# Optimization experiments

Measured on AMD Instinct MI355X. Metric: run time of the kernel, lower is better.

Reference implementation:

```python
import jax, jax.numpy as jnp
import numpy as np

T, N, H, G = 4, 100000, 128, 1024
LN2 = float(np.log(2.0))
EPS = 1e-5


def ssp(x):
    # shifted softplus: softplus(x) - softplus(0)
    return jax.nn.softplus(x) - LN2


def layernorm(x, g, b):
    m = jnp.mean(x, axis=-1, keepdims=True)
    v = jnp.var(x, axis=-1, keepdims=True)
    return (x - m) * jax.lax.rsqrt(v + EPS) * g + b


def mlp3(x, Ws, bs, gs, bts):
    # 3 stacked Linear -> LayerNorm -> SSP stages
    for i in range(3):
        x = ssp(layernorm(x @ Ws[i] + bs[i], gs[i], bts[i]))
    return x


def setup_inputs() -> dict:
    key = jax.random.key(0)
    ks = jax.random.split(key, 8)
    s = 1.0 / np.sqrt(H)
    batch = jnp.sort((jnp.arange(N, dtype=jnp.int64) * G) // N).astype(jnp.int32)
    return {
        "x_proc": jax.random.normal(ks[0], (T, N, H), jnp.float32),
        "x_enc": jax.random.normal(ks[1], (N, H), jnp.float32),
        "batch": batch,
        "pW": jax.random.normal(ks[2], (3, H, H), jnp.float32) * s,
        "pb": jnp.zeros((3, H), jnp.float32),
        "pg": jnp.ones((3, H), jnp.float32),
        "pbt": jnp.zeros((3, H), jnp.float32),
        "eW": jax.random.normal(ks[3], (3, H, H), jnp.float32) * s,
        "eb": jnp.zeros((3, H), jnp.float32),
        "eg": jnp.ones((3, H), jnp.float32),
        "ebt": jnp.zeros((3, H), jnp.float32),
        "wp": jax.random.normal(ks[4], (H, 1), jnp.float32) * s,
        "bp": jnp.zeros((1,), jnp.float32),
        "we": jax.random.normal(ks[5], (H, 1), jnp.float32) * s,
        "be": jnp.zeros((1,), jnp.float32),
    }


def reference(x_proc, x_enc, batch, pW, pb, pg, pbt, eW, eb, eg, ebt, wp, bp, we, be):
    h_proc = mlp3(x_proc, pW, pb, pg, pbt)          # [T, N, H]
    h_enc = mlp3(x_enc, eW, eb, eg, ebt)            # [N, H]
    seg = lambda z: jax.ops.segment_sum(z, batch, num_segments=G)
    pooled_proc = jax.vmap(seg)(h_proc)             # [T, G, H]
    pooled_enc = seg(h_enc)                         # [G, H]
    target = pooled_proc @ wp + bp + (pooled_enc @ we + be)[None]  # [T, G, 1]
    return target.reshape(-1, G)                    # [T, G]
```

## Files before the change

### kernel.cpp

```cpp
#include <hip/hip_runtime.h>
#include <hip/hip_bf16.h>

typedef unsigned short u16;
typedef unsigned int u32;
typedef __bf16 bf16x8 __attribute__((ext_vector_type(8)));
typedef float f32x16 __attribute__((ext_vector_type(16)));
typedef float f32x4 __attribute__((ext_vector_type(4)));
typedef u32 u32x4 __attribute__((ext_vector_type(4)));

typedef __attribute__((address_space(1))) const u32 glb_u32;
typedef __attribute__((address_space(3))) u32 lds_u32;

#define NN 100000
#define NPROC_BLOCKS 3125
#define NENC_BLOCKS 782
#define LN2F 0.69314718055994530942f
#define LOG2EF 1.44269504088896340736f
#define CSTRIDE 1284

__device__ __forceinline__ u16 f2bf(float f) {
  u32 u = __float_as_uint(f);
  u32 r = u + 0x7fffu + ((u >> 16) & 1u);
  return (u16)(r >> 16);
}

__device__ __forceinline__ u32 pk2(float a, float b) {
  float2 f2; f2.x = a; f2.y = b;
  __hip_bfloat162 h = __float22bfloat162_rn(f2);
  u32 r;
  __builtin_memcpy(&r, &h, 4);
  return r;
}

__device__ __forceinline__ float l2p1e(float xp) {
  return __builtin_amdgcn_logf(1.0f + __builtin_amdgcn_exp2f(xp));
}

__global__ void prep_kernel(const float* __restrict__ pW, const float* __restrict__ eW,
                            const float* __restrict__ pb, const float* __restrict__ pg,
                            const float* __restrict__ pbt,
                            const float* __restrict__ eb, const float* __restrict__ eg,
                            const float* __restrict__ ebt,
                            const float* __restrict__ wp, const float* __restrict__ we,
                            const float* __restrict__ bp, const float* __restrict__ be,
                            u16* __restrict__ wt, float* __restrict__ cprep,
                            float* __restrict__ out) {
  int bx = blockIdx.x;
  int t = threadIdx.x;
  if (bx < 384) {
    int idx = bx * 256 + t;
    int m = idx >> 14;
    int within = idx & 16383;
    int r = within >> 7;
    int c = within & 127;
    int k = (((c >> 3) ^ (r & 15)) << 3) | (c & 7);
    const float* src = (m < 3) ? pW : eW;
    int ms = (m < 3) ? m : m - 3;
    float w = src[ms * 16384 + k * 128 + r];
    if (ms >= 1) w *= LN2F;
    wt[idx] = f2bf(w);
    if (idx < 4096) out[idx] = bp[0] + be[0];
  } else {
    int net = bx - 384;
    const float* W  = net ? eW : pW;
    const float* b  = net ? eb : pb;
    const float* g  = net ? eg : pg;
    const float* bt = net ? ebt : pbt;
    const float* wv = net ? we : wp;
    float* cp = cprep + net * CSTRIDE;
    if (t < 128) {
      int j = t;
      #pragma unroll
      for (int s = 0; s < 3; ++s) {
        float bb = b[s * 128 + j];
        if (s >= 1) {
          float cs = 0.f;
          #pragma unroll 8
          for (int k = 0; k < 128; ++k) cs += W[s * 16384 + k * 128 + j];
          bb -= LN2F * cs;
        }
        cp[(s * 3 + 0) * 128 + j] = bb;
        cp[(s * 3 + 1) * 128 + j] = g[s * 128 + j] * LOG2EF;
        cp[(s * 3 + 2) * 128 + j] = bt[s * 128 + j] * LOG2EF;
      }
      cp[9 * 128 + j] = LN2F * wv[j];
    }
    if (t == 0) {
      float ssum = 0.f;
      #pragma unroll 8
      for (int j = 0; j < 128; ++j) ssum += wv[j];
      cp[1280] = -LN2F * ssum;
    }
  }
}

__global__ __launch_bounds__(256, 4)
void mlp_kernel(const float* __restrict__ x_proc, const float* __restrict__ x_enc,
                const u16* __restrict__ wt, const float* __restrict__ cprep,
                const int* __restrict__ batch, float* __restrict__ out) {
  __shared__ __align__(16) unsigned char wbuf[32768];
  __shared__ f32x4 cball[10][32];
  __shared__ float c0s;

  const bool is_proc = blockIdx.x < NPROC_BLOCKS;
  const int bid2 = is_proc ? blockIdx.x : blockIdx.x - NPROC_BLOCKS;
  const float* x = is_proc ? x_proc : x_enc;
  const unsigned char* wgb = (const unsigned char*)(is_proc ? wt : wt + 49152);
  const float* cp = cprep + (is_proc ? 0 : CSTRIDE);
  const int nrows = is_proc ? 400000 : 100000;

  const int tid = threadIdx.x;
  const int lane = tid & 63;
  const int wid = tid >> 6;
  const int l31 = lane & 31;
  const u32 hi = (u32)(lane >> 5);
  const int brow = bid2 * 128;

  auto issue_w = [&](int s_) {
    #pragma unroll
    for (int i = 0; i < 8; ++i) {
      const unsigned char* gp = wgb + s_ * 32768 + i * 4096 + tid * 16;
      unsigned char* lp = wbuf + i * 4096 + wid * 1024;
      __builtin_amdgcn_global_load_lds((const glb_u32*)(const void*)gp,
                                       (lds_u32*)(void*)lp, 16, 0, 0);
    }
  };

  issue_w(0);

  for (int i = tid; i < 320; i += 256)
    ((f32x4*)cball)[i] = *(const f32x4*)(cp + i * 4);
  if (tid == 0) c0s = cp[1280];

  const int rloc = wid * 32 + l31;
  const int grow = brow + rloc;
  const float* xr = x + (size_t)((grow < nrows) ? grow : (nrows - 1)) * 128 + (int)hi * 8;
  bf16x8 bfr[8];
  #pragma unroll
  for (int half = 0; half < 2; ++half) {
    f32x4 a[8];
    #pragma unroll
    for (int k4 = 0; k4 < 4; ++k4) {
      a[2 * k4]     = *(const f32x4*)(xr + (half * 4 + k4) * 16);
      a[2 * k4 + 1] = *(const f32x4*)(xr + (half * 4 + k4) * 16 + 4);
    }
    #pragma unroll
    for (int k4 = 0; k4 < 4; ++k4) {
      u32x4 tq;
      tq.x = pk2(a[2 * k4][0], a[2 * k4][1]);
      tq.y = pk2(a[2 * k4][2], a[2 * k4][3]);
      tq.z = pk2(a[2 * k4 + 1][0], a[2 * k4 + 1][1]);
      tq.w = pk2(a[2 * k4 + 1][2], a[2 * k4 + 1][3]);
      bfr[half * 4 + k4] = __builtin_bit_cast(bf16x8, tq);
    }
    __builtin_amdgcn_sched_barrier(0);
  }

  float pfin = 0.0f;

  #pragma unroll
  for (int s = 0; s < 3; ++s) {
    __syncthreads();

    f32x16 acc[4];
    #pragma unroll
    for (int jf = 0; jf < 4; ++jf)
      #pragma unroll
      for (int q = 0; q < 4; ++q) {
        f32x4 b4 = cball[s * 3 + 0][jf * 8 + 2 * q + (int)hi];
        acc[jf][4 * q + 0] = b4[0];
        acc[jf][4 * q + 1] = b4[1];
        acc[jf][4 * q + 2] = b4[2];
        acc[jf][4 * q + 3] = b4[3];
      }

    #pragma unroll
    for (int ks = 0; ks < 8; ++ks) {
      int aoff = l31 * 256 + (((2 * ks + (int)hi) ^ (l31 & 15)) << 4);
      #pragma unroll
      for (int jf = 0; jf < 4; ++jf) {
        const bf16x8 afrag = *(const bf16x8*)(const void*)(wbuf + jf * 8192 + aoff);
        acc[jf] = __builtin_amdgcn_mfma_f32_32x32x16_bf16(afrag, bfr[ks], acc[jf], 0, 0, 0);
      }
    }

    if (s < 2) {
      __syncthreads();
      issue_w(s + 1);
    }

    float s1 = 0.f, s2 = 0.f;
    #pragma unroll
    for (int jf = 0; jf < 4; ++jf) {
      float p1 = 0.f, p2 = 0.f;
      #pragma unroll
      for (int e = 0; e < 16; ++e) {
        float v = acc[jf][e];
        p1 += v;
        p2 = __builtin_fmaf(v, v, p2);
      }
      s1 += p1; s2 += p2;
    }
    s1 += __shfl_xor(s1, 32, 64);
    s2 += __shfl_xor(s2, 32, 64);
    float mean = s1 * 0.0078125f;
    float var = s2 * 0.0078125f - mean * mean;
    float rstd = rsqrtf(var + 1e-5f);
    float nmr = -mean * rstd;

    if (s < 2) {
      #pragma unroll
      for (int ks = 0; ks < 8; ++ks) {
        int jf = ks >> 1, q0 = (ks & 1) << 1;
        uint2 wq[2];
        #pragma unroll
        for (int qq = 0; qq < 2; ++qq) {
          int q = q0 + qq;
          f32x4 g4 = cball[s * 3 + 1][jf * 8 + 2 * q + (int)hi];
          f32x4 t4 = cball[s * 3 + 2][jf * 8 + 2 * q + (int)hi];
          float r0 = l2p1e((acc[jf][4 * q + 0] * rstd + nmr) * g4[0] + t4[0]);
          float r1 = l2p1e((acc[jf][4 * q + 1] * rstd + nmr) * g4[1] + t4[1]);
          float r2 = l2p1e((acc[jf][4 * q + 2] * rstd + nmr) * g4[2] + t4[2]);
          float r3 = l2p1e((acc[jf][4 * q + 3] * rstd + nmr) * g4[3] + t4[3]);
          wq[qq].x = pk2(r0, r1);
          wq[qq].y = pk2(r2, r3);
        }
        u32 sx = hi ? wq[0].x : wq[1].x;
        u32 sy = hi ? wq[0].y : wq[1].y;
        u32 rx = (u32)__shfl_xor((int)sx, 32, 64);
        u32 ry = (u32)__shfl_xor((int)sy, 32, 64);
        u32x4 tq;
        tq.x = hi ? rx : wq[0].x;
        tq.y = hi ? ry : wq[0].y;
        tq.z = hi ? wq[1].x : rx;
        tq.w = hi ? wq[1].y : ry;
        bfr[ks] = __builtin_bit_cast(bf16x8, tq);
      }
    } else {
      float p = 0.f;
      #pragma unroll
      for (int jf = 0; jf < 4; ++jf)
        #pragma unroll
        for (int q = 0; q < 4; ++q) {
          f32x4 g4 = cball[7][jf * 8 + 2 * q + (int)hi];
          f32x4 t4 = cball[8][jf * 8 + 2 * q + (int)hi];
          f32x4 w4 = cball[9][jf * 8 + 2 * q + (int)hi];
          #pragma unroll
          for (int e = 0; e < 4; ++e) {
            float v = l2p1e((acc[jf][4 * q + e] * rstd + nmr) * g4[e] + t4[e]);
            p = __builtin_fmaf(v, w4[e], p);
          }
        }
      pfin = p;
    }
  }

  pfin += __shfl_xor(pfin, 32, 64);
  if (grow < nrows) {
    pfin += c0s;
    int cell;
    if (is_proc) {
      int tt = grow / NN;
      cell = tt * 1024 + batch[grow - tt * NN];
    } else {
      cell = batch[grow];
    }
    int ca = __shfl(cell, 0, 32);
    int cz = __shfl(cell, 31, 32);
    if (ca == cz) {
      float r = pfin;
      #pragma unroll
      for (int off = 1; off < 32; off <<= 1) r += __shfl_xor(r, off, 64);
      if (hi == 0) {
        if (is_proc) {
          if (l31 == 0) atomicAdd(out + ca, r);
        } else {
          if (l31 < 4) atomicAdd(out + l31 * 1024 + ca, r);
        }
      }
    } else if (hi == 0) {
      if (is_proc) {
        atomicAdd(out + cell, pfin);
      } else {
        #pragma unroll
        for (int t2 = 0; t2 < 4; ++t2) atomicAdd(out + t2 * 1024 + cell, pfin);
      }
    }
  }
}

extern "C" void kernel_launch(void* const* d_in, const int* in_sizes, int n_in,
                              void* d_out, int out_size, void* d_ws, size_t ws_size,
                              hipStream_t stream) {
  const float* x_proc = (const float*)d_in[0];
  const float* x_enc  = (const float*)d_in[1];
  const int*   batch  = (const int*)d_in[2];
  const float* pW  = (const float*)d_in[3];
  const float* pb  = (const float*)d_in[4];
  const float* pg  = (const float*)d_in[5];
  const float* pbt = (const float*)d_in[6];
  const float* eW  = (const float*)d_in[7];
  const float* eb  = (const float*)d_in[8];
  const float* eg  = (const float*)d_in[9];
  const float* ebt = (const float*)d_in[10];
  const float* wp  = (const float*)d_in[11];
  const float* bp  = (const float*)d_in[12];
  const float* we  = (const float*)d_in[13];
  const float* be  = (const float*)d_in[14];

  float* out = (float*)d_out;
  u16* wt_ws = (u16*)d_ws;
  float* cprep = (float*)((char*)d_ws + 196608);

  prep_kernel<<<386, 256, 0, stream>>>(pW, eW, pb, pg, pbt, eb, eg, ebt,
                                       wp, we, bp, be, wt_ws, cprep, out);
  mlp_kernel<<<NPROC_BLOCKS + NENC_BLOCKS, 256, 0, stream>>>(
      x_proc, x_enc, wt_ws, cprep, batch, out);
}
```

Measured before the change: 154.3 us.

## Recompute per-fragment MFMAs to cut accumulator registers and double-buffer activations

Each layer's GEMM is now split per output fragment. The statistics pass computes one 32x32 accumulator at a time, and the normalize pass recomputes the MFMAs instead of keeping all four accumulators live. The bf16 activation fragments are double-buffered so the next layer's inputs can be written while the current ones are still read. The weight-prefetch barrier is moved to after the last two fragments are recomputed. This cuts VGPR pressure and may raise occupancy, but it roughly doubles MFMA and LDS weight-read work per layer.

New measurement: 158.4 us. 2.7% more time.

```diff
diff --git a/kernel.cpp b/kernel.cpp
--- a/kernel.cpp
+++ b/kernel.cpp
@@ -135,67 +135,93 @@
   const int rloc = wid * 32 + l31;
   const int grow = brow + rloc;
   const float* xr = x + (size_t)((grow < nrows) ? grow : (nrows - 1)) * 128 + (int)hi * 8;
-  bf16x8 bfr[8];
+  bf16x8 bfr[2][8];
   #pragma unroll
-  for (int half = 0; half < 2; ++half) {
-    f32x4 a[8];
-    #pragma unroll
-    for (int k4 = 0; k4 < 4; ++k4) {
-      a[2 * k4]     = *(const f32x4*)(xr + (half * 4 + k4) * 16);
-      a[2 * k4 + 1] = *(const f32x4*)(xr + (half * 4 + k4) * 16 + 4);
-    }
-    #pragma unroll
-    for (int k4 = 0; k4 < 4; ++k4) {
+  for (int c4 = 0; c4 < 4; ++c4) {
+    f32x4 a[4];
+    #pragma unroll
+    for (int k2 = 0; k2 < 2; ++k2) {
+      a[2 * k2]     = *(const f32x4*)(xr + (c4 * 2 + k2) * 16);
+      a[2 * k2 + 1] = *(const f32x4*)(xr + (c4 * 2 + k2) * 16 + 4);
+    }
+    #pragma unroll
+    for (int k2 = 0; k2 < 2; ++k2) {
       u32x4 tq;
-      tq.x = pk2(a[2 * k4][0], a[2 * k4][1]);
-      tq.y = pk2(a[2 * k4][2], a[2 * k4][3]);
-      tq.z = pk2(a[2 * k4 + 1][0], a[2 * k4 + 1][1]);
-      tq.w = pk2(a[2 * k4 + 1][2], a[2 * k4 + 1][3]);
-      bfr[half * 4 + k4] = __builtin_bit_cast(bf16x8, tq);
+      tq.x = pk2(a[2 * k2][0], a[2 * k2][1]);
+      tq.y = pk2(a[2 * k2][2], a[2 * k2][3]);
+      tq.z = pk2(a[2 * k2 + 1][0], a[2 * k2 + 1][1]);
+      tq.w = pk2(a[2 * k2 + 1][2], a[2 * k2 + 1][3]);
+      bfr[0][c4 * 2 + k2] = __builtin_bit_cast(bf16x8, tq);
     }
     __builtin_amdgcn_sched_barrier(0);
   }
 
+  auto mfma_jf = [&](int s_, int jf, const bf16x8* bc) -> f32x16 {
+    f32x16 a;
+    #pragma unroll
+    for (int q = 0; q < 4; ++q) {
+      f32x4 b4 = cball[s_ * 3 + 0][jf * 8 + 2 * q + (int)hi];
+      a[4 * q + 0] = b4[0];
+      a[4 * q + 1] = b4[1];
+      a[4 * q + 2] = b4[2];
+      a[4 * q + 3] = b4[3];
+    }
+    #pragma unroll
+    for (int ks = 0; ks < 8; ++ks) {
+      int aoff = l31 * 256 + (((2 * ks + (int)hi) ^ (l31 & 15)) << 4);
+      const bf16x8 afrag = *(const bf16x8*)(const void*)(wbuf + jf * 8192 + aoff);
+      a = __builtin_amdgcn_mfma_f32_32x32x16_bf16(afrag, bc[ks], a, 0, 0, 0);
+    }
+    return a;
+  };
+
+  auto norm_ex = [&](int s_, int jf, const f32x16& a, float rstd, float nmr,
+                     bf16x8* bn) {
+    #pragma unroll
+    for (int half = 0; half < 2; ++half) {
+      uint2 wq[2];
+      #pragma unroll
+      for (int qq = 0; qq < 2; ++qq) {
+        int q = half * 2 + qq;
+        f32x4 g4 = cball[s_ * 3 + 1][jf * 8 + 2 * q + (int)hi];
+        f32x4 t4 = cball[s_ * 3 + 2][jf * 8 + 2 * q + (int)hi];
+        float r0 = l2p1e((a[4 * q + 0] * rstd + nmr) * g4[0] + t4[0]);
+        float r1 = l2p1e((a[4 * q + 1] * rstd + nmr) * g4[1] + t4[1]);
+        float r2 = l2p1e((a[4 * q + 2] * rstd + nmr) * g4[2] + t4[2]);
+        float r3 = l2p1e((a[4 * q + 3] * rstd + nmr) * g4[3] + t4[3]);
+        wq[qq].x = pk2(r0, r1);
+        wq[qq].y = pk2(r2, r3);
+      }
+      u32 sx = hi ? wq[0].x : wq[1].x;
+      u32 sy = hi ? wq[0].y : wq[1].y;
+      u32 rx = (u32)__shfl_xor((int)sx, 32, 64);
+      u32 ry = (u32)__shfl_xor((int)sy, 32, 64);
+      u32x4 tq;
+      tq.x = hi ? rx : wq[0].x;
+      tq.y = hi ? ry : wq[0].y;
+      tq.z = hi ? wq[1].x : rx;
+      tq.w = hi ? wq[1].y : ry;
+      bn[2 * jf + half] = __builtin_bit_cast(bf16x8, tq);
+    }
+  };
+
   float pfin = 0.0f;
 
   #pragma unroll
   for (int s = 0; s < 3; ++s) {
+    const bf16x8* bc = bfr[s & 1];
+    bf16x8* bn = bfr[(s & 1) ^ 1];
+
     __syncthreads();
 
-    f32x16 acc[4];
-    #pragma unroll
-    for (int jf = 0; jf < 4; ++jf)
-      #pragma unroll
-      for (int q = 0; q < 4; ++q) {
-        f32x4 b4 = cball[s * 3 + 0][jf * 8 + 2 * q + (int)hi];
-        acc[jf][4 * q + 0] = b4[0];
-        acc[jf][4 * q + 1] = b4[1];
-        acc[jf][4 * q + 2] = b4[2];
-        acc[jf][4 * q + 3] = b4[3];
-      }
-
-    #pragma unroll
-    for (int ks = 0; ks < 8; ++ks) {
-      int aoff = l31 * 256 + (((2 * ks + (int)hi) ^ (l31 & 15)) << 4);
-      #pragma unroll
-      for (int jf = 0; jf < 4; ++jf) {
-        const bf16x8 afrag = *(const bf16x8*)(const void*)(wbuf + jf * 8192 + aoff);
-        acc[jf] = __builtin_amdgcn_mfma_f32_32x32x16_bf16(afrag, bfr[ks], acc[jf], 0, 0, 0);
-      }
-    }
-
-    if (s < 2) {
-      __syncthreads();
-      issue_w(s + 1);
-    }
-
     float s1 = 0.f, s2 = 0.f;
     #pragma unroll
     for (int jf = 0; jf < 4; ++jf) {
+      f32x16 a = mfma_jf(s, jf, bc);
       float p1 = 0.f, p2 = 0.f;
       #pragma unroll
       for (int e = 0; e < 16; ++e) {
-        float v = acc[jf][e];
+        float v = a[e];
         p1 += v;
         p2 = __builtin_fmaf(v, v, p2);
       }
@@ -210,36 +236,21 @@
 
     if (s < 2) {
       #pragma unroll
-      for (int ks = 0; ks < 8; ++ks) {
-        int jf = ks >> 1, q0 = (ks & 1) << 1;
-        uint2 wq[2];
-        #pragma unroll
-        for (int qq = 0; qq < 2; ++qq) {
-          int q = q0 + qq;
-          f32x4 g4 = cball[s * 3 + 1][jf * 8 + 2 * q + (int)hi];
-          f32x4 t4 = cball[s * 3 + 2][jf * 8 + 2 * q + (int)hi];
-          float r0 = l2p1e((acc[jf][4 * q + 0] * rstd + nmr) * g4[0] + t4[0]);
-          float r1 = l2p1e((acc[jf][4 * q + 1] * rstd + nmr) * g4[1] + t4[1]);
-          float r2 = l2p1e((acc[jf][4 * q + 2] * rstd + nmr) * g4[2] + t4[2]);
-          float r3 = l2p1e((acc[jf][4 * q + 3] * rstd + nmr) * g4[3] + t4[3]);
-          wq[qq].x = pk2(r0, r1);
-          wq[qq].y = pk2(r2, r3);
-        }
-        u32 sx = hi ? wq[0].x : wq[1].x;
-        u32 sy = hi ? wq[0].y : wq[1].y;
-        u32 rx = (u32)__shfl_xor((int)sx, 32, 64);
-        u32 ry = (u32)__shfl_xor((int)sy, 32, 64);
-        u32x4 tq;
-        tq.x = hi ? rx : wq[0].x;
-        tq.y = hi ? ry : wq[0].y;
-        tq.z = hi ? wq[1].x : rx;
-        tq.w = hi ? wq[1].y : ry;
-        bfr[ks] = __builtin_bit_cast(bf16x8, tq);
-      }
+      for (int jf = 0; jf < 2; ++jf) {
+        f32x16 a = mfma_jf(s, jf, bc);
+        norm_ex(s, jf, a, rstd, nmr, bn);
+      }
+      f32x16 a2 = mfma_jf(s, 2, bc);
+      f32x16 a3 = mfma_jf(s, 3, bc);
+      __syncthreads();
+      issue_w(s + 1);
+      norm_ex(s, 2, a2, rstd, nmr, bn);
+      norm_ex(s, 3, a3, rstd, nmr, bn);
     } else {
       float p = 0.f;
       #pragma unroll
-      for (int jf = 0; jf < 4; ++jf)
+      for (int jf = 0; jf < 4; ++jf) {
+        f32x16 a = mfma_jf(s, jf, bc);
         #pragma unroll
         for (int q = 0; q < 4; ++q) {
           f32x4 g4 = cball[7][jf * 8 + 2 * q + (int)hi];
@@ -247,10 +258,11 @@
           f32x4 w4 = cball[9][jf * 8 + 2 * q + (int)hi];
           #pragma unroll
           for (int e = 0; e < 4; ++e) {
-            float v = l2p1e((acc[jf][4 * q + e] * rstd + nmr) * g4[e] + t4[e]);
+            float v = l2p1e((a[4 * q + e] * rstd + nmr) * g4[e] + t4[e]);
             p = __builtin_fmaf(v, w4[e], p);
           }
         }
+      }
       pfin = p;
     }
   }
```
